# Kernel tuning notes

Hardware: AMD Instinct MI355X
Metric: run time of the kernel (lower is better)

## Reference

```python
import jax, jax.numpy as jnp
import numpy as np

GRAD_WIDTH = 0.5  # PeriodicExponential defaults in sinabs
GRAD_SCALE = 1.0

B, T, C_IN, C_OUT = 100, 500, 300, 500


def setup_inputs() -> dict:
    key = jax.random.key(0)
    k1, k2, k3 = jax.random.split(key, 3)
    x = jax.random.normal(k1, (B, T, C_IN), dtype=jnp.float32)
    W = jax.random.normal(k2, (C_OUT, C_IN), dtype=jnp.float32) / np.sqrt(C_IN).astype(np.float32)
    alpha = jax.random.uniform(k3, (B * C_OUT,), dtype=jnp.float32)  # decay in [0,1)
    return {"x": x, "W": W, "alpha": alpha}


def _periodic_exp_pdf(v_mem, threshold):
    # sinabs.activation.PeriodicExponential surrogate gradient
    vs = v_mem - threshold / 2
    vper = vs - threshold * jnp.floor(vs / threshold)
    vnew = jnp.where(v_mem < threshold, vs, vper)
    return GRAD_SCALE / GRAD_WIDTH * jnp.exp(-jnp.abs(vnew - threshold / 2) / GRAD_WIDTH)


@jax.custom_vjp
def spike_fn(v_pre, threshold):
    # multi-spike: floor(v/theta) spikes when above threshold (max_num_spikes=None)
    return jnp.where(v_pre >= threshold, jnp.floor(v_pre / threshold), 0.0)


def _spike_fwd(v_pre, threshold):
    return spike_fn(v_pre, threshold), (v_pre, threshold)


def _spike_bwd(res, g):
    v_pre, threshold = res
    return (g * _periodic_exp_pdf(v_pre, threshold), jnp.zeros_like(threshold))


spike_fn.defvjp(_spike_fwd, _spike_bwd)


def _lif_forward(x, W, alpha):
    threshold = jnp.ones_like(alpha)
    v_init = jnp.zeros_like(alpha)
    # Linear (no bias): [B,T,Cin] @ [Cout,Cin]^T -> [B,T,Cout]
    x_lin = jnp.einsum('btc,oc->bto', x, W)
    # movedim(1,-1).flatten(0,1) -> neurons [B*Cout], time-major for scan: [T, B*Cout]
    inp = x_lin.transpose(1, 0, 2).reshape(T, B * C_OUT)

    def step(v, x_t):
        v_pre = alpha * v + x_t                      # leaky integrate
        v_pre = jnp.maximum(v_pre, -threshold)       # lower bound min_v_mem = -threshold
        s = spike_fn(v_pre, threshold)               # fire (multi-spike)
        v_post = v_pre - threshold * s               # reset by membrane subtraction
        return v_post, s

    _, spikes = jax.lax.scan(step, v_init, inp)      # spikes: [T, B*Cout]
    # reshape(B, Cout, T).movedim(-1, 1) -> [B, T, Cout]
    return spikes.reshape(T, B, C_OUT).transpose(1, 0, 2)


def reference(x, W, alpha):
    return _lif_forward(x, W, alpha)
```

## Files before the change

### kernel.cpp

```cpp
#include <hip/hip_runtime.h>
#include <hip/hip_bf16.h>

#define NB 100
#define NT 500
#define CIN 300
#define COUT 500
#define M_TOT (NB * NT)

constexpr int BM = 128, BN = 128, BK = 32;
constexpr int LDA = BM + 4;

__global__ __launch_bounds__(256) void gemm_f32(
    const float* __restrict__ X, const float* __restrict__ W, float* __restrict__ C)
{
    __shared__ float As[BK][LDA];
    __shared__ float Bs[BK][LDA];

    const int ntiles_n = (COUT + BN - 1) / BN;
    const int mtile = blockIdx.x / ntiles_n;
    const int ntile = blockIdx.x % ntiles_n;
    const int m0 = mtile * BM, n0 = ntile * BN;

    const int tid  = threadIdx.x;
    const int lane = tid & 63;
    const int wid  = tid >> 6;
    const int wmb  = (wid >> 1) << 6;
    const int wnb  = (wid & 1) << 6;
    const int r4   = (lane >> 3) << 2;
    const int c4   = (lane & 7) << 2;

    const int lr = tid >> 3;
    const int lk = (tid & 7) << 2;

    float acc[8][8];
    #pragma unroll
    for (int i = 0; i < 8; ++i)
        #pragma unroll
        for (int j = 0; j < 8; ++j) acc[i][j] = 0.f;

    for (int k0 = 0; k0 < CIN; k0 += BK) {
        const int kk = k0 + lk;
        const bool kv = (kk < CIN);
        #pragma unroll
        for (int p = 0; p < 4; ++p) {
            int row = p * 32 + lr;
            int m = m0 + row;
            float4 v = make_float4(0.f, 0.f, 0.f, 0.f);
            if (kv && m < M_TOT) v = *(const float4*)(X + (size_t)m * CIN + kk);
            As[lk + 0][row] = v.x; As[lk + 1][row] = v.y;
            As[lk + 2][row] = v.z; As[lk + 3][row] = v.w;
        }
        #pragma unroll
        for (int p = 0; p < 4; ++p) {
            int row = p * 32 + lr;
            int o = n0 + row;
            float4 v = make_float4(0.f, 0.f, 0.f, 0.f);
            if (kv && o < COUT) v = *(const float4*)(W + (size_t)o * CIN + kk);
            Bs[lk + 0][row] = v.x; Bs[lk + 1][row] = v.y;
            Bs[lk + 2][row] = v.z; Bs[lk + 3][row] = v.w;
        }
        __syncthreads();
        #pragma unroll 8
        for (int k = 0; k < BK; ++k) {
            float4 a0 = *(const float4*)&As[k][wmb + r4];
            float4 a1 = *(const float4*)&As[k][wmb + 32 + r4];
            float4 b0 = *(const float4*)&Bs[k][wnb + c4];
            float4 b1 = *(const float4*)&Bs[k][wnb + 32 + c4];
            float a[8] = {a0.x, a0.y, a0.z, a0.w, a1.x, a1.y, a1.z, a1.w};
            float b[8] = {b0.x, b0.y, b0.z, b0.w, b1.x, b1.y, b1.z, b1.w};
            #pragma unroll
            for (int i = 0; i < 8; ++i)
                #pragma unroll
                for (int j = 0; j < 8; ++j)
                    acc[i][j] += a[i] * b[j];
        }
        __syncthreads();
    }

    #pragma unroll
    for (int h = 0; h < 2; ++h) {
        #pragma unroll
        for (int i = 0; i < 4; ++i) {
            const int m = m0 + wmb + h * 32 + r4 + i;
            if (m >= M_TOT) continue;
            float* cp = C + (size_t)m * COUT;
            const int col0 = n0 + wnb + c4;
            const int col1 = col0 + 32;
            const int ai = h * 4 + i;
            if (col0 < COUT)
                *(float4*)(cp + col0) = make_float4(acc[ai][0], acc[ai][1], acc[ai][2], acc[ai][3]);
            if (col1 < COUT)
                *(float4*)(cp + col1) = make_float4(acc[ai][4], acc[ai][5], acc[ai][6], acc[ai][7]);
        }
    }
}

__global__ __launch_bounds__(256) void lif_scan(
    const float* __restrict__ alpha, float* __restrict__ C)
{
    const int n = blockIdx.x * blockDim.x + threadIdx.x;
    if (n >= NB * COUT) return;
    const int b = n / COUT, o = n % COUT;
    const float a = alpha[n];
    float v = 0.f;
    float* p = C + (size_t)b * NT * COUT + o;

    constexpr int U = 10;
    for (int t0 = 0; t0 < NT; t0 += U) {
        float xl[U];
        #pragma unroll
        for (int u = 0; u < U; ++u) xl[u] = p[(size_t)(t0 + u) * COUT];
        float s[U];
        #pragma unroll
        for (int u = 0; u < U; ++u) {
            float vp = a * v + xl[u];
            vp = fmaxf(vp, -1.f);
            float sp = (vp >= 1.f) ? floorf(vp) : 0.f;
            v = vp - sp;
            s[u] = sp;
        }
        #pragma unroll
        for (int u = 0; u < U; ++u) p[(size_t)(t0 + u) * COUT] = s[u];
    }
}

extern "C" void kernel_launch(void* const* d_in, const int* in_sizes, int n_in,
                              void* d_out, int out_size, void* d_ws, size_t ws_size,
                              hipStream_t stream) {
    const float* X     = (const float*)d_in[0];
    const float* W     = (const float*)d_in[1];
    const float* alpha = (const float*)d_in[2];
    float* C = (float*)d_out;

    const int mtiles = (M_TOT + BM - 1) / BM;
    const int ntiles = (COUT + BN - 1) / BN;
    gemm_f32<<<dim3(mtiles * ntiles), dim3(256), 0, stream>>>(X, W, C);

    const int nneur = NB * COUT;
    lif_scan<<<dim3((nneur + 255) / 256), dim3(256), 0, stream>>>(alpha, C);
}
```

Measured before the change: 272.0 us.

## Double-buffer GEMM shared-memory tiles with register prefetch of next K slice

```diff
diff --git a/kernel.cpp b/kernel.cpp
--- a/kernel.cpp
+++ b/kernel.cpp
@@ -7,14 +7,15 @@
 #define COUT 500
 #define M_TOT (NB * NT)
 
-constexpr int BM = 128, BN = 128, BK = 32;
+constexpr int BM = 128, BN = 128, BK = 16;
 constexpr int LDA = BM + 4;
+constexpr int NSTEP = (CIN + BK - 1) / BK;
 
 __global__ __launch_bounds__(256) void gemm_f32(
     const float* __restrict__ X, const float* __restrict__ W, float* __restrict__ C)
 {
-    __shared__ float As[BK][LDA];
-    __shared__ float Bs[BK][LDA];
+    __shared__ float As[2][BK][LDA];
+    __shared__ float Bs[2][BK][LDA];
 
     const int ntiles_n = (COUT + BN - 1) / BN;
     const int mtile = blockIdx.x / ntiles_n;
@@ -29,8 +30,17 @@
     const int r4   = (lane >> 3) << 2;
     const int c4   = (lane & 7) << 2;
 
-    const int lr = tid >> 3;
-    const int lk = (tid & 7) << 2;
+    const int srow = tid >> 1;
+    const int sq0  = (tid & 1) * 2;
+
+    const int mr = min(m0 + srow, M_TOT - 1);
+    const int orr = min(n0 + srow, COUT - 1);
+    const float* xp = X + (size_t)mr * CIN;
+    const float* wp = W + (size_t)orr * CIN;
+
+    auto ldq = [](const float* p, int kk) -> float4 {
+        return (kk < CIN) ? *(const float4*)(p + kk) : make_float4(0.f, 0.f, 0.f, 0.f);
+    };
 
     float acc[8][8];
     #pragma unroll
@@ -38,34 +48,42 @@
         #pragma unroll
         for (int j = 0; j < 8; ++j) acc[i][j] = 0.f;
 
-    for (int k0 = 0; k0 < CIN; k0 += BK) {
-        const int kk = k0 + lk;
-        const bool kv = (kk < CIN);
+    float4 xa0 = ldq(xp, sq0 * 4);
+    float4 xa1 = ldq(xp, sq0 * 4 + 4);
+    float4 wb0 = ldq(wp, sq0 * 4);
+    float4 wb1 = ldq(wp, sq0 * 4 + 4);
+
+    #define WRITE_TILE(buf)                                                     \
+        do {                                                                    \
+            As[buf][sq0 * 4 + 0][srow] = xa0.x; As[buf][sq0 * 4 + 1][srow] = xa0.y; \
+            As[buf][sq0 * 4 + 2][srow] = xa0.z; As[buf][sq0 * 4 + 3][srow] = xa0.w; \
+            As[buf][sq0 * 4 + 4][srow] = xa1.x; As[buf][sq0 * 4 + 5][srow] = xa1.y; \
+            As[buf][sq0 * 4 + 6][srow] = xa1.z; As[buf][sq0 * 4 + 7][srow] = xa1.w; \
+            Bs[buf][sq0 * 4 + 0][srow] = wb0.x; Bs[buf][sq0 * 4 + 1][srow] = wb0.y; \
+            Bs[buf][sq0 * 4 + 2][srow] = wb0.z; Bs[buf][sq0 * 4 + 3][srow] = wb0.w; \
+            Bs[buf][sq0 * 4 + 4][srow] = wb1.x; Bs[buf][sq0 * 4 + 5][srow] = wb1.y; \
+            Bs[buf][sq0 * 4 + 6][srow] = wb1.z; Bs[buf][sq0 * 4 + 7][srow] = wb1.w; \
+        } while (0)
+
+    WRITE_TILE(0);
+    __syncthreads();
+
+    int cur = 0;
+    for (int step = 0; step < NSTEP; ++step) {
+        if (step + 1 < NSTEP) {
+            const int kn = (step + 1) * BK + sq0 * 4;
+            xa0 = ldq(xp, kn);
+            xa1 = ldq(xp, kn + 4);
+            wb0 = ldq(wp, kn);
+            wb1 = ldq(wp, kn + 4);
+        }
+
         #pragma unroll
-        for (int p = 0; p < 4; ++p) {
-            int row = p * 32 + lr;
-            int m = m0 + row;
-            float4 v = make_float4(0.f, 0.f, 0.f, 0.f);
-            if (kv && m < M_TOT) v = *(const float4*)(X + (size_t)m * CIN + kk);
-            As[lk + 0][row] = v.x; As[lk + 1][row] = v.y;
-            As[lk + 2][row] = v.z; As[lk + 3][row] = v.w;
-        }
-        #pragma unroll
-        for (int p = 0; p < 4; ++p) {
-            int row = p * 32 + lr;
-            int o = n0 + row;
-            float4 v = make_float4(0.f, 0.f, 0.f, 0.f);
-            if (kv && o < COUT) v = *(const float4*)(W + (size_t)o * CIN + kk);
-            Bs[lk + 0][row] = v.x; Bs[lk + 1][row] = v.y;
-            Bs[lk + 2][row] = v.z; Bs[lk + 3][row] = v.w;
-        }
-        __syncthreads();
-        #pragma unroll 8
         for (int k = 0; k < BK; ++k) {
-            float4 a0 = *(const float4*)&As[k][wmb + r4];
-            float4 a1 = *(const float4*)&As[k][wmb + 32 + r4];
-            float4 b0 = *(const float4*)&Bs[k][wnb + c4];
-            float4 b1 = *(const float4*)&Bs[k][wnb + 32 + c4];
+            float4 a0 = *(const float4*)&As[cur][k][wmb + r4];
+            float4 a1 = *(const float4*)&As[cur][k][wmb + 32 + r4];
+            float4 b0 = *(const float4*)&Bs[cur][k][wnb + c4];
+            float4 b1 = *(const float4*)&Bs[cur][k][wnb + 32 + c4];
             float a[8] = {a0.x, a0.y, a0.z, a0.w, a1.x, a1.y, a1.z, a1.w};
             float b[8] = {b0.x, b0.y, b0.z, b0.w, b1.x, b1.y, b1.z, b1.w};
             #pragma unroll
@@ -74,7 +92,12 @@
                 for (int j = 0; j < 8; ++j)
                     acc[i][j] += a[i] * b[j];
         }
-        __syncthreads();
+
+        if (step + 1 < NSTEP) {
+            WRITE_TILE(cur ^ 1);
+            __syncthreads();
+            cur ^= 1;
+        }
     }
 
     #pragma unroll
@@ -93,6 +116,7 @@
                 *(float4*)(cp + col1) = make_float4(acc[ai][4], acc[ai][5], acc[ai][6], acc[ai][7]);
         }
     }
+    #undef WRITE_TILE
 }
 
 __global__ __launch_bounds__(256) void lif_scan(
```

Result: slower. 370.0 us (+36.0%).

## Pre-transpose GEMM operands into K-major panels and double-buffer via direct LDS loads

Applied to the files above, without the earlier changes.

```diff
diff --git a/kernel.cpp b/kernel.cpp
--- a/kernel.cpp
+++ b/kernel.cpp
@@ -1,25 +1,62 @@
 #include <hip/hip_runtime.h>
 #include <hip/hip_bf16.h>
+#include <stdint.h>
 
 #define NB 100
 #define NT 500
 #define CIN 300
 #define COUT 500
 #define M_TOT (NB * NT)
-
-constexpr int BM = 128, BN = 128, BK = 32;
-constexpr int LDA = BM + 4;
-
-__global__ __launch_bounds__(256) void gemm_f32(
-    const float* __restrict__ X, const float* __restrict__ W, float* __restrict__ C)
-{
-    __shared__ float As[BK][LDA];
-    __shared__ float Bs[BK][LDA];
-
-    const int ntiles_n = (COUT + BN - 1) / BN;
-    const int mtile = blockIdx.x / ntiles_n;
-    const int ntile = blockIdx.x % ntiles_n;
-    const int m0 = mtile * BM, n0 = ntile * BN;
+#define MTILES 391
+#define NTILES 4
+#define KTILES 10
+#define NPANEL (MTILES * KTILES + NTILES * KTILES)
+#define WS_NEED ((size_t)NPANEL * 4096 * 4)
+
+__device__ __forceinline__ void gload_lds16(const void* g, void* l) {
+    __builtin_amdgcn_global_load_lds(
+        (const __attribute__((address_space(1))) unsigned int*)g,
+        (__attribute__((address_space(3))) unsigned int*)l,
+        16, 0, 0);
+}
+
+__global__ __launch_bounds__(256) void split_t(
+    const float* __restrict__ X, const float* __restrict__ W, float* __restrict__ ws)
+{
+    const int bid = blockIdx.x;
+    const int tid = threadIdx.x;
+    const float* src; int rowbase, nrows, kt;
+    if (bid < MTILES * KTILES) {
+        src = X; rowbase = (bid / KTILES) * 128; nrows = M_TOT; kt = bid % KTILES;
+    } else {
+        const int w = bid - MTILES * KTILES;
+        src = W; rowbase = (w / KTILES) * 128; nrows = COUT; kt = w % KTILES;
+    }
+    const int kk = tid >> 3;
+    const int m0 = (tid & 7) * 16;
+    const int k  = kt * 32 + kk;
+
+    float v[16];
+    #pragma unroll
+    for (int j = 0; j < 16; ++j) {
+        const int row = rowbase + m0 + j;
+        v[j] = (row < nrows && k < CIN) ? src[(size_t)row * CIN + k] : 0.f;
+    }
+    float* out = ws + (size_t)bid * 4096 + (size_t)kk * 128 + m0;
+    #pragma unroll
+    for (int c = 0; c < 4; ++c)
+        *(float4*)(out + c * 4) = make_float4(v[c*4], v[c*4+1], v[c*4+2], v[c*4+3]);
+}
+
+__global__ __launch_bounds__(256) void gemm_t(
+    const float* __restrict__ ws, float* __restrict__ C)
+{
+    __shared__ __align__(16) float As[2][32][128];
+    __shared__ __align__(16) float Bs[2][32][128];
+
+    const int mtile = blockIdx.x >> 2;
+    const int ntile = blockIdx.x & 3;
+    const int m0 = mtile * 128, n0 = ntile * 128;
 
     const int tid  = threadIdx.x;
     const int lane = tid & 63;
@@ -29,6 +66,87 @@
     const int r4   = (lane >> 3) << 2;
     const int c4   = (lane & 7) << 2;
 
+    const float* Xp = ws + (size_t)(mtile * KTILES) * 4096;
+    const float* Wp = ws + (size_t)(MTILES * KTILES + ntile * KTILES) * 4096;
+
+    float acc[8][8];
+    #pragma unroll
+    for (int i = 0; i < 8; ++i)
+        #pragma unroll
+        for (int j = 0; j < 8; ++j) acc[i][j] = 0.f;
+
+    auto stage = [&](int buf, int kt) {
+        const float* xs = Xp + (size_t)kt * 4096 + tid * 4;
+        const float* wsr = Wp + (size_t)kt * 4096 + tid * 4;
+        #pragma unroll
+        for (int c = 0; c < 4; ++c) {
+            gload_lds16(xs + c * 1024, (char*)&As[buf][0][0] + (c * 256 + tid) * 16);
+            gload_lds16(wsr + c * 1024, (char*)&Bs[buf][0][0] + (c * 256 + tid) * 16);
+        }
+    };
+
+    stage(0, 0);
+    __syncthreads();
+
+    for (int kt = 0; kt < KTILES; ++kt) {
+        const int cur = kt & 1;
+        if (kt + 1 < KTILES) stage(cur ^ 1, kt + 1);
+
+        #pragma unroll 8
+        for (int k = 0; k < 32; ++k) {
+            float4 a0 = *(const float4*)&As[cur][k][wmb + r4];
+            float4 a1 = *(const float4*)&As[cur][k][wmb + 32 + r4];
+            float4 b0 = *(const float4*)&Bs[cur][k][wnb + c4];
+            float4 b1 = *(const float4*)&Bs[cur][k][wnb + 32 + c4];
+            float a[8] = {a0.x, a0.y, a0.z, a0.w, a1.x, a1.y, a1.z, a1.w};
+            float b[8] = {b0.x, b0.y, b0.z, b0.w, b1.x, b1.y, b1.z, b1.w};
+            #pragma unroll
+            for (int i = 0; i < 8; ++i)
+                #pragma unroll
+                for (int j = 0; j < 8; ++j)
+                    acc[i][j] += a[i] * b[j];
+        }
+        __syncthreads();
+    }
+
+    #pragma unroll
+    for (int h = 0; h < 2; ++h) {
+        #pragma unroll
+        for (int i = 0; i < 4; ++i) {
+            const int m = m0 + wmb + h * 32 + r4 + i;
+            if (m >= M_TOT) continue;
+            float* cp = C + (size_t)m * COUT;
+            const int col0 = n0 + wnb + c4;
+            const int col1 = col0 + 32;
+            const int ai = h * 4 + i;
+            if (col0 < COUT)
+                *(float4*)(cp + col0) = make_float4(acc[ai][0], acc[ai][1], acc[ai][2], acc[ai][3]);
+            if (col1 < COUT)
+                *(float4*)(cp + col1) = make_float4(acc[ai][4], acc[ai][5], acc[ai][6], acc[ai][7]);
+        }
+    }
+}
+
+constexpr int BM = 128, BN = 128, BK = 32;
+constexpr int LDA = BM + 4;
+
+__global__ __launch_bounds__(256) void gemm_f32(
+    const float* __restrict__ X, const float* __restrict__ W, float* __restrict__ C)
+{
+    __shared__ float As[BK][LDA];
+    __shared__ float Bs[BK][LDA];
+
+    const int mtile = blockIdx.x >> 2;
+    const int ntile = blockIdx.x & 3;
+    const int m0 = mtile * BM, n0 = ntile * BN;
+
+    const int tid  = threadIdx.x;
+    const int lane = tid & 63;
+    const int wid  = tid >> 6;
+    const int wmb  = (wid >> 1) << 6;
+    const int wnb  = (wid & 1) << 6;
+    const int r4   = (lane >> 3) << 2;
+    const int c4   = (lane & 7) << 2;
     const int lr = tid >> 3;
     const int lk = (tid & 7) << 2;
 
@@ -132,9 +250,13 @@
     const float* alpha = (const float*)d_in[2];
     float* C = (float*)d_out;
 
-    const int mtiles = (M_TOT + BM - 1) / BM;
-    const int ntiles = (COUT + BN - 1) / BN;
-    gemm_f32<<<dim3(mtiles * ntiles), dim3(256), 0, stream>>>(X, W, C);
+    if (ws_size >= WS_NEED && d_ws != nullptr) {
+        float* ws = (float*)d_ws;
+        split_t<<<dim3(NPANEL), dim3(256), 0, stream>>>(X, W, ws);
+        gemm_t<<<dim3(MTILES * NTILES), dim3(256), 0, stream>>>(ws, C);
+    } else {
+        gemm_f32<<<dim3(MTILES * NTILES), dim3(256), 0, stream>>>(X, W, C);
+    }
 
     const int nneur = NB * COUT;
     lif_scan<<<dim3((nneur + 255) / 256), dim3(256), 0, stream>>>(alpha, C);
```

New measurement: 293.8 us. 8.0% more time.
